# Performance work log

Measured on AMD Instinct MI355X. Metric: run time of the kernel, lower is better.

## Reference

```python
import jax, jax.numpy as jnp
import numpy as np

B, LA, LB = 16, 2048, 2048
DA, DB, DH = 768, 512, 512
EPS = 1e-5


def _layer_norm(x, g, b):
    mu = jnp.mean(x, axis=-1, keepdims=True)
    var = jnp.var(x, axis=-1, keepdims=True)
    return (x - mu) * jax.lax.rsqrt(var + EPS) * g + b


def setup_inputs() -> dict:
    key = jax.random.key(0)
    ks = jax.random.split(key, 12)
    s = lambda d: 1.0 / np.sqrt(d)
    return {
        "z_a": jax.random.normal(ks[0], (B, LA, DA), jnp.float32),
        "z_b": jax.random.normal(ks[1], (B, LB, DB), jnp.float32),
        "Wa": jax.random.uniform(ks[2], (DA, DH), jnp.float32, -s(DA), s(DA)),
        "ba": jnp.zeros((DH,), jnp.float32),
        "Wb": jax.random.uniform(ks[3], (DB, DH), jnp.float32, -s(DB), s(DB)),
        "bb": jnp.zeros((DH,), jnp.float32),
        "W_co": jax.random.normal(ks[4], (DH, DH), jnp.float32),
        "Woa": jax.random.uniform(ks[5], (DH, DA), jnp.float32, -s(DH), s(DH)),
        "boa": jnp.zeros((DA,), jnp.float32),
        "Wob": jax.random.uniform(ks[6], (DH, DB), jnp.float32, -s(DH), s(DH)),
        "bob": jnp.zeros((DB,), jnp.float32),
        "ga": jnp.ones((DA,), jnp.float32),
        "beta_a": jnp.zeros((DA,), jnp.float32),
        "gb": jnp.ones((DB,), jnp.float32),
        "beta_b": jnp.zeros((DB,), jnp.float32),
    }


def reference(z_a, z_b, Wa, ba, Wb, bb, W_co, Woa, boa, Wob, bob, ga, beta_a, gb, beta_b):
    # projections to shared hidden space
    h_a = jnp.einsum('bld,dh->blh', z_a, Wa) + ba          # (B, LA, DH)
    h_b = jnp.einsum('bld,dh->blh', z_b, Wb) + bb          # (B, LB, DH)
    # bilinear tanh co-attention scores
    C = jnp.tanh(jnp.einsum('bih,hk,bjk->bij', h_a, W_co, h_b))  # (B, LA, LB)
    attn_a = jax.nn.softmax(C, axis=-1)                    # rows: over LB
    attn_b = jax.nn.softmax(C.transpose(0, 2, 1), axis=-1) # cols: over LA
    h_a_co = jnp.einsum('bij,bjh->bih', attn_a, h_b)       # (B, LA, DH)
    h_b_co = jnp.einsum('bji,bih->bjh', attn_b, h_a)       # (B, LB, DH)
    z_a_co = jnp.einsum('blh,hd->bld', h_a_co, Woa) + boa
    z_b_co = jnp.einsum('blh,hd->bld', h_b_co, Wob) + bob
    z_a_out = _layer_norm(z_a + z_a_co, ga, beta_a)
    z_b_out = _layer_norm(z_b + z_b_co, gb, beta_b)
    return (z_a_out, z_b_out)
```

## Files before the change

kernel.cpp:

```cpp
#include <hip/hip_runtime.h>
#include <stdint.h>

typedef short bf16x8 __attribute__((ext_vector_type(8)));
typedef float f32x4 __attribute__((ext_vector_type(4)));

#define BM 256
#define BN 256
#define BK 64
#define ABUF_U 16384
#define BUF_U  32768

#define AS1 __attribute__((address_space(1)))
#define AS3 __attribute__((address_space(3)))

__device__ __forceinline__ ushort f2bf(float x) {
    uint32_t u = __float_as_uint(x);
    u += 0x7FFFu + ((u >> 16) & 1u);
    return (ushort)(u >> 16);
}

__device__ __forceinline__ void gload16(const void* g, void* l) {
    __builtin_amdgcn_global_load_lds((const AS1 void*)g, (AS3 void*)l, 16, 0, 0);
}

#define ISSUE2(kt, buf, i0)                                                          \
    do {                                                                             \
        gload16(((i0) < 4 ? Ap : Bp) + goff[i0] + (kt), smem + (buf)*BUF_U + loff[i0]); \
        gload16((((i0)+1) < 4 ? Ap : Bp) + goff[(i0)+1] + (kt), smem + (buf)*BUF_U + loff[(i0)+1]); \
    } while (0)

template<int MODE, bool HAS_BIAS, bool WRITE_T>
__global__ __launch_bounds__(512, 2)
void gemm_bt(const ushort* __restrict__ Aptr_, const ushort* __restrict__ Bptr_,
             void* __restrict__ Cptr_, ushort* __restrict__ CTptr_,
             const float* __restrict__ bias, const float* __restrict__ resid_,
             float* __restrict__ rsum_, float* __restrict__ csum_,
             const float* __restrict__ scale_,
             int M, int N, int K, int lda, int ldb, int ldc,
             long sA, long sB, long sC, long sCT, long sSum,
             int ldct, int rbshift)
{
    extern __shared__ ushort smem[];

    const int z    = blockIdx.z;
    const int m0   = blockIdx.x * BM;
    const int n0   = blockIdx.y * BN;
    const int tid  = threadIdx.x;
    const int lane = tid & 63;
    const int wave = tid >> 6;
    const int wr   = wave >> 2;
    const int wcn  = wave & 3;
    const int g    = lane >> 4, c = lane & 15;

    const ushort* Ap = Aptr_ + z * sA;
    const ushort* Bp = Bptr_ + z * sB;

    long goff[8]; int loff[8];
    #pragma unroll
    for (int u = 0; u < 4; ++u) {
        const int li  = u * 512 + tid;
        const int row = li >> 3;
        const int gck = (li & 7) ^ (row & 7);
        goff[u]     = (long)(m0 + row) * lda + gck * 8;
        loff[u]     = li * 8;
        goff[u + 4] = (long)(n0 + row) * ldb + gck * 8;
        loff[u + 4] = ABUF_U + li * 8;
    }

    f32x4 acc[8][4] = {};

    const int nk = K / BK;
    ISSUE2(0, 0, 0); ISSUE2(0, 0, 2); ISSUE2(0, 0, 4); ISSUE2(0, 0, 6);

    for (int t = 0; t < nk; ++t) {
        const int cur = t & 1, nxt = cur ^ 1;
        const ushort* As = smem + cur * BUF_U;
        const ushort* Bs = As + ABUF_U;
        const bool pf = (t + 1 < nk);
        const int kt1 = (t + 1) * BK;

        if (pf) {
            ISSUE2(kt1, nxt, 0);
            asm volatile("s_waitcnt vmcnt(2)" ::: "memory");
        } else {
            asm volatile("s_waitcnt vmcnt(0)" ::: "memory");
        }
        __builtin_amdgcn_s_barrier();

        bf16x8 af[8], bfr2[2];

        auto ldA = [&](int kk) {
            #pragma unroll
            for (int mi = 0; mi < 8; ++mi) {
                const int row = wr * 128 + mi * 16 + c;
                const int ckq = (kk * 4 + g) ^ (row & 7);
                af[mi] = *(const bf16x8*)&As[row * BK + ckq * 8];
            }
        };
        auto ldB = [&](int kk, int nh) {
            #pragma unroll
            for (int u = 0; u < 2; ++u) {
                const int row = wcn * 64 + (nh * 2 + u) * 16 + c;
                const int ckq = (kk * 4 + g) ^ (row & 7);
                bfr2[u] = *(const bf16x8*)&Bs[row * BK + ckq * 8];
            }
        };
        auto mm = [&](int nh) {
            __builtin_amdgcn_s_setprio(1);
            #pragma unroll
            for (int mi = 0; mi < 8; ++mi)
                #pragma unroll
                for (int u = 0; u < 2; ++u)
                    acc[mi][nh * 2 + u] = __builtin_amdgcn_mfma_f32_16x16x32_bf16(
                        af[mi], bfr2[u], acc[mi][nh * 2 + u], 0, 0, 0);
            __builtin_amdgcn_s_setprio(0);
        };

        ldA(0); ldB(0, 0);
        if (pf) ISSUE2(kt1, nxt, 2);
        __builtin_amdgcn_s_barrier();
        asm volatile("s_waitcnt lgkmcnt(0)" ::: "memory");
        __builtin_amdgcn_sched_barrier(0);
        mm(0);
        __builtin_amdgcn_s_barrier();
        ldB(0, 1);
        if (pf) ISSUE2(kt1, nxt, 4);
        __builtin_amdgcn_s_barrier();
        asm volatile("s_waitcnt lgkmcnt(0)" ::: "memory");
        __builtin_amdgcn_sched_barrier(0);
        mm(1);
        __builtin_amdgcn_s_barrier();
        ldA(1); ldB(1, 0);
        if (pf) ISSUE2(kt1, nxt, 6);
        __builtin_amdgcn_s_barrier();
        asm volatile("s_waitcnt lgkmcnt(0)" ::: "memory");
        __builtin_amdgcn_sched_barrier(0);
        mm(0);
        __builtin_amdgcn_s_barrier();
        ldB(1, 1);
        __builtin_amdgcn_s_barrier();
        asm volatile("s_waitcnt lgkmcnt(0)" ::: "memory");
        __builtin_amdgcn_sched_barrier(0);
        mm(1);
        __builtin_amdgcn_s_barrier();
    }

    if constexpr (MODE == 0) {
        ushort* Cp = (ushort*)Cptr_ + z * sC;
        #pragma unroll
        for (int mi = 0; mi < 8; ++mi) {
            const int row = m0 + wr * 128 + mi * 16 + g * 4;
            #pragma unroll
            for (int ni = 0; ni < 4; ++ni) {
                const int col = n0 + wcn * 64 + ni * 16 + c;
                const float bv = HAS_BIAS ? bias[col] : 0.f;
                ushort v[4];
                #pragma unroll
                for (int r = 0; r < 4; ++r) v[r] = f2bf(acc[mi][ni][r] + bv);
                #pragma unroll
                for (int r = 0; r < 4; ++r) Cp[(long)(row + r) * ldc + col] = v[r];
                if constexpr (WRITE_T) {
                    const int bb = row >> rbshift;
                    const int ii = row & ((1 << rbshift) - 1);
                    *(ushort4*)&CTptr_[(long)bb * sCT + (long)col * ldct + ii] =
                        make_ushort4(v[0], v[1], v[2], v[3]);
                }
            }
        }
    } else if constexpr (MODE == 1) {
        ushort* Ep  = (ushort*)Cptr_ + z * sC;
        ushort* ETp = CTptr_ + z * sCT;
        float* rs = rsum_ + z * sSum;
        float* cs = csum_ + z * sSum;
        float rowpart[8][4] = {};
        float colpart[4] = {};
        #pragma unroll
        for (int mi = 0; mi < 8; ++mi) {
            const int row = m0 + wr * 128 + mi * 16 + g * 4;
            #pragma unroll
            for (int ni = 0; ni < 4; ++ni) {
                const int col = n0 + wcn * 64 + ni * 16 + c;
                ushort v[4];
                #pragma unroll
                for (int r = 0; r < 4; ++r) {
                    const float s = acc[mi][ni][r];
                    const float t = 1.f - 2.f / (__expf(2.f * s) + 1.f);
                    const float e = __expf(t);
                    rowpart[mi][r] += e;
                    colpart[ni]    += e;
                    v[r] = f2bf(e);
                }
                #pragma unroll
                for (int r = 0; r < 4; ++r) Ep[(long)(row + r) * ldc + col] = v[r];
                *(ushort4*)&ETp[(long)col * ldct + row] = make_ushort4(v[0], v[1], v[2], v[3]);
            }
        }
        #pragma unroll
        for (int mi = 0; mi < 8; ++mi) {
            #pragma unroll
            for (int r = 0; r < 4; ++r) {
                float v = rowpart[mi][r];
                v += __shfl_xor(v, 1); v += __shfl_xor(v, 2);
                v += __shfl_xor(v, 4); v += __shfl_xor(v, 8);
                if (c == 0) atomicAdd(&rs[m0 + wr * 128 + mi * 16 + g * 4 + r], v);
            }
        }
        #pragma unroll
        for (int ni = 0; ni < 4; ++ni) {
            float v = colpart[ni];
            v += __shfl_xor(v, 16); v += __shfl_xor(v, 32);
            if (g == 0) atomicAdd(&cs[n0 + wcn * 64 + ni * 16 + c], v);
        }
    } else if constexpr (MODE == 2) {
        const float* sc = scale_ + z * sSum;
        ushort* Cp = (ushort*)Cptr_ + z * sC;
        #pragma unroll
        for (int mi = 0; mi < 8; ++mi) {
            const int row = m0 + wr * 128 + mi * 16 + g * 4;
            float rcp[4];
            #pragma unroll
            for (int r = 0; r < 4; ++r) rcp[r] = 1.f / sc[row + r];
            #pragma unroll
            for (int ni = 0; ni < 4; ++ni) {
                const int col = n0 + wcn * 64 + ni * 16 + c;
                #pragma unroll
                for (int r = 0; r < 4; ++r)
                    Cp[(long)(row + r) * ldc + col] = f2bf(acc[mi][ni][r] * rcp[r]);
            }
        }
    } else {
        float* Co = (float*)Cptr_;
        #pragma unroll
        for (int mi = 0; mi < 8; ++mi) {
            const int row = m0 + wr * 128 + mi * 16 + g * 4;
            #pragma unroll
            for (int ni = 0; ni < 4; ++ni) {
                const int col = n0 + wcn * 64 + ni * 16 + c;
                const float bv = bias[col];
                #pragma unroll
                for (int r = 0; r < 4; ++r) {
                    const long idx = (long)(row + r) * ldc + col;
                    Co[idx] = acc[mi][ni][r] + bv + resid_[idx];
                }
            }
        }
    }
}

__global__ __launch_bounds__(256)
void cast32to16(const float* __restrict__ in, ushort* __restrict__ out, long n) {
    const long stride = (long)gridDim.x * 256 * 8;
    for (long i = ((long)blockIdx.x * 256 + threadIdx.x) * 8; i < n; i += stride) {
        const float4 f0 = *(const float4*)(in + i);
        const float4 f1 = *(const float4*)(in + i + 4);
        uint4 w;
        w.x = (uint)f2bf(f0.x) | ((uint)f2bf(f0.y) << 16);
        w.y = (uint)f2bf(f0.z) | ((uint)f2bf(f0.w) << 16);
        w.z = (uint)f2bf(f1.x) | ((uint)f2bf(f1.y) << 16);
        w.w = (uint)f2bf(f1.z) | ((uint)f2bf(f1.w) << 16);
        *(uint4*)(out + i) = w;
    }
}

__global__ __launch_bounds__(256)
void tcast(const float* __restrict__ in, ushort* __restrict__ out, int R, int C) {
    __shared__ float t[32][33];
    const int bx = blockIdx.x * 32, by = blockIdx.y * 32;
    const int tx = threadIdx.x, ty = threadIdx.y;
    for (int i = ty; i < 32; i += 8) {
        const int r = by + i, cc = bx + tx;
        if (r < R && cc < C) t[i][tx] = in[(long)r * C + cc];
    }
    __syncthreads();
    for (int i = ty; i < 32; i += 8) {
        const int cc = bx + i, r = by + tx;
        if (cc < C && r < R) out[(long)cc * R + r] = f2bf(t[tx][i]);
    }
}

template<int D>
__global__ __launch_bounds__(256)
void ln_rows(float* __restrict__ y, const float* __restrict__ gam, const float* __restrict__ bet) {
    constexpr int NV = D / 256;
    const long row = blockIdx.x;
    float* p = y + row * D;
    const int tid = threadIdx.x;
    float v[NV];
    float s = 0.f, s2 = 0.f;
    #pragma unroll
    for (int k = 0; k < NV; ++k) {
        v[k] = p[tid + k * 256];
        s += v[k]; s2 += v[k] * v[k];
    }
    #pragma unroll
    for (int off = 1; off < 64; off <<= 1) {
        s  += __shfl_xor(s, off);
        s2 += __shfl_xor(s2, off);
    }
    __shared__ float ws[4], ws2[4];
    const int wave = tid >> 6, lane = tid & 63;
    if (lane == 0) { ws[wave] = s; ws2[wave] = s2; }
    __syncthreads();
    s  = ws[0] + ws[1] + ws[2] + ws[3];
    s2 = ws2[0] + ws2[1] + ws2[2] + ws2[3];
    const float mu  = s / D;
    const float var = s2 / D - mu * mu;
    const float rstd = rsqrtf(var + 1e-5f);
    #pragma unroll
    for (int k = 0; k < NV; ++k) {
        const int i = tid + k * 256;
        p[i] = (v[k] - mu) * rstd * gam[i] + bet[i];
    }
}

extern "C" void kernel_launch(void* const* d_in, const int* in_sizes, int n_in,
                              void* d_out, int out_size, void* d_ws, size_t ws_size,
                              hipStream_t stream)
{
    (void)in_sizes; (void)n_in; (void)out_size; (void)ws_size;
    const float* z_a    = (const float*)d_in[0];
    const float* z_b    = (const float*)d_in[1];
    const float* Wa     = (const float*)d_in[2];
    const float* ba     = (const float*)d_in[3];
    const float* Wb     = (const float*)d_in[4];
    const float* bb     = (const float*)d_in[5];
    const float* Wco    = (const float*)d_in[6];
    const float* Woa    = (const float*)d_in[7];
    const float* boa    = (const float*)d_in[8];
    const float* Wob    = (const float*)d_in[9];
    const float* bob    = (const float*)d_in[10];
    const float* ga     = (const float*)d_in[11];
    const float* beta_a = (const float*)d_in[12];
    const float* gb     = (const float*)d_in[13];
    const float* beta_b = (const float*)d_in[14];

    const int Bn = 16, LA = 2048, LB = 2048, DA = 768, DB = 512, DH = 512;
    const long MA = (long)Bn * LA;
    const long MB = (long)Bn * LB;

    char* w = (char*)d_ws;
    size_t off = 0;
    auto alc = [&](size_t bytes) { void* p = w + off; off += (bytes + 255) & ~(size_t)255; return p; };

    ushort* WaT  = (ushort*)alc((size_t)DH * DA * 2);
    ushort* WbT  = (ushort*)alc((size_t)DH * DB * 2);
    ushort* WcoT = (ushort*)alc((size_t)DH * DH * 2);
    ushort* WoaT = (ushort*)alc((size_t)DA * DH * 2);
    ushort* WobT = (ushort*)alc((size_t)DB * DH * 2);
    ushort* h_a  = (ushort*)alc((size_t)MA * DH * 2);
    ushort* h_b  = (ushort*)alc((size_t)MB * DH * 2);
    ushort* h_aT = (ushort*)alc((size_t)Bn * DH * LA * 2);
    ushort* h_bT = (ushort*)alc((size_t)Bn * DH * LB * 2);
    ushort* Ma   = (ushort*)alc((size_t)MA * DH * 2);
    ushort* E    = (ushort*)alc((size_t)Bn * LA * LB * 2);
    ushort* ET   = (ushort*)alc((size_t)Bn * LB * LA * 2);
    ushort* Pa   = (ushort*)alc((size_t)MA * DH * 2);
    ushort* Pb   = (ushort*)alc((size_t)MB * DH * 2);
    float*  rsum = (float*)alc((size_t)Bn * LA * 4);
    float*  csum = (float*)alc((size_t)Bn * LB * 4);

    ushort* za16 = E;
    ushort* zb16 = E + (size_t)MA * DA;

    dim3 blk(512, 1, 1);
    dim3 blk256(256, 1, 1);
    dim3 tb(32, 8, 1);
    const int SHM = 2 * BUF_U * 2;

    tcast<<<dim3(DH / 32, DA / 32, 1), tb, 0, stream>>>(Wa,  WaT,  DA, DH);
    tcast<<<dim3(DH / 32, DB / 32, 1), tb, 0, stream>>>(Wb,  WbT,  DB, DH);
    tcast<<<dim3(DH / 32, DH / 32, 1), tb, 0, stream>>>(Wco, WcoT, DH, DH);
    tcast<<<dim3(DA / 32, DH / 32, 1), tb, 0, stream>>>(Woa, WoaT, DH, DA);
    tcast<<<dim3(DB / 32, DH / 32, 1), tb, 0, stream>>>(Wob, WobT, DH, DB);

    cast32to16<<<dim3(2048, 1, 1), blk256, 0, stream>>>(z_a, za16, MA * DA);
    cast32to16<<<dim3(2048, 1, 1), blk256, 0, stream>>>(z_b, zb16, MB * DB);

    hipMemsetAsync(rsum, 0, (size_t)Bn * (LA + LB) * sizeof(float), stream);

    gemm_bt<0, true, true><<<dim3(MA / BM, DH / BN, 1), blk, SHM, stream>>>(
        za16, WaT, h_a, h_aT, ba, nullptr, nullptr, nullptr, nullptr,
        (int)MA, DH, DA, DA, DA, DH, 0, 0, 0, (long)DH * LA, 0, LA, 11);

    gemm_bt<0, true, true><<<dim3(MB / BM, DH / BN, 1), blk, SHM, stream>>>(
        zb16, WbT, h_b, h_bT, bb, nullptr, nullptr, nullptr, nullptr,
        (int)MB, DH, DB, DB, DB, DH, 0, 0, 0, (long)DH * LB, 0, LB, 11);

    gemm_bt<0, false, false><<<dim3(MA / BM, DH / BN, 1), blk, SHM, stream>>>(
        h_a, WcoT, Ma, nullptr, nullptr, nullptr, nullptr, nullptr, nullptr,
        (int)MA, DH, DH, DH, DH, DH, 0, 0, 0, 0, 0, 0, 0);

    gemm_bt<1, false, false><<<dim3(LA / BM, LB / BN, Bn), blk, SHM, stream>>>(
        Ma, h_b, E, ET, nullptr, nullptr, rsum, csum, nullptr,
        LA, LB, DH, DH, DH, LB,
        (long)LA * DH, (long)LB * DH, (long)LA * LB, (long)LB * LA, LA, LA, 0);

    gemm_bt<2, false, false><<<dim3(LA / BM, DH / BN, Bn), blk, SHM, stream>>>(
        E, h_bT, Pa, nullptr, nullptr, nullptr, nullptr, nullptr, rsum,
        LA, DH, LB, LB, LB, DH,
        (long)LA * LB, (long)DH * LB, (long)LA * DH, 0, LA, 0, 0);

    gemm_bt<2, false, false><<<dim3(LB / BM, DH / BN, Bn), blk, SHM, stream>>>(
        ET, h_aT, Pb, nullptr, nullptr, nullptr, nullptr, nullptr, csum,
        LB, DH, LA, LA, LA, DH,
        (long)LB * LA, (long)DH * LA, (long)LB * DH, 0, LB, 0, 0);

    float* outA = (float*)d_out;
    float* outB = outA + MA * DA;

    gemm_bt<3, true, false><<<dim3(MA / BM, DA / BN, 1), blk, SHM, stream>>>(
        Pa, WoaT, outA, nullptr, boa, z_a, nullptr, nullptr, nullptr,
        (int)MA, DA, DH, DH, DH, DA, 0, 0, 0, 0, 0, 0, 0);

    gemm_bt<3, true, false><<<dim3(MB / BM, DB / BN, 1), blk, SHM, stream>>>(
        Pb, WobT, outB, nullptr, bob, z_b, nullptr, nullptr, nullptr,
        (int)MB, DB, DH, DH, DH, DB, 0, 0, 0, 0, 0, 0, 0);

    ln_rows<768><<<dim3((unsigned)MA, 1, 1), blk256, 0, stream>>>(outA, ga, beta_a);
    ln_rows<512><<<dim3((unsigned)MB, 1, 1), blk256, 0, stream>>>(outB, gb, beta_b);
}
```

Baseline: 719.9 us.

## Stage GEMM epilogues through swizzled LDS for coalesced 16-byte global stores

All epilogue modes now write accumulator tiles into XOR-swizzled shared memory, then read them back row-contiguously and issue 16-byte vector stores. The transposed outputs are staged the same way, and the fp32 output in mode 3 uses float4 loads of bias and residual. This replaces scattered 2-byte and 4-byte global stores, including the strided transposed writes, with coalesced ones. The cost is extra LDS traffic and barriers, and the LDS buffer is reused across two halves of the tile in mode 3.

After: 726.5 us. No clear change (+0.9%).

```diff
diff --git a/kernel.cpp b/kernel.cpp
--- a/kernel.cpp
+++ b/kernel.cpp
@@ -145,103 +145,157 @@
         __builtin_amdgcn_s_barrier();
     }
 
-    if constexpr (MODE == 0) {
-        ushort* Cp = (ushort*)Cptr_ + z * sC;
+    char* img = (char*)smem;
+
+    if constexpr (MODE == 3) {
+        float* Co = (float*)Cptr_;
         #pragma unroll
-        for (int mi = 0; mi < 8; ++mi) {
-            const int row = m0 + wr * 128 + mi * 16 + g * 4;
-            #pragma unroll
-            for (int ni = 0; ni < 4; ++ni) {
-                const int col = n0 + wcn * 64 + ni * 16 + c;
-                const float bv = HAS_BIAS ? bias[col] : 0.f;
-                ushort v[4];
-                #pragma unroll
-                for (int r = 0; r < 4; ++r) v[r] = f2bf(acc[mi][ni][r] + bv);
-                #pragma unroll
-                for (int r = 0; r < 4; ++r) Cp[(long)(row + r) * ldc + col] = v[r];
-                if constexpr (WRITE_T) {
-                    const int bb = row >> rbshift;
-                    const int ii = row & ((1 << rbshift) - 1);
-                    *(ushort4*)&CTptr_[(long)bb * sCT + (long)col * ldct + ii] =
-                        make_ushort4(v[0], v[1], v[2], v[3]);
+        for (int h = 0; h < 2; ++h) {
+            if (h) __syncthreads();
+            if (wr == h) {
+                #pragma unroll
+                for (int mi = 0; mi < 8; ++mi) {
+                    const int lr0 = mi * 16 + g * 4;
+                    const int s3  = ((lr0 >> 2) & 7) << 4;
+                    #pragma unroll
+                    for (int ni = 0; ni < 4; ++ni) {
+                        const int lc4 = (wcn * 64 + ni * 16 + c) * 4;
+                        #pragma unroll
+                        for (int r = 0; r < 4; ++r)
+                            *(float*)(img + (lr0 + r) * 1024 + (lc4 ^ s3)) = acc[mi][ni][r];
+                    }
                 }
             }
-        }
-    } else if constexpr (MODE == 1) {
-        ushort* Ep  = (ushort*)Cptr_ + z * sC;
-        ushort* ETp = CTptr_ + z * sCT;
-        float* rs = rsum_ + z * sSum;
-        float* cs = csum_ + z * sSum;
+            __syncthreads();
+            #pragma unroll
+            for (int cc = 0; cc < 16; ++cc) {
+                const int ch = cc * 512 + tid;
+                const int rl = ch >> 6;
+                const int cb = (ch & 63) * 16;
+                const int s3 = ((rl >> 2) & 7) << 4;
+                float4 v = *(const float4*)(img + rl * 1024 + (cb ^ s3));
+                const int col = n0 + (ch & 63) * 4;
+                const int row = m0 + h * 128 + rl;
+                const float4 bv = *(const float4*)&bias[col];
+                const float4 rv = *(const float4*)&resid_[(long)row * ldc + col];
+                v.x += bv.x + rv.x; v.y += bv.y + rv.y;
+                v.z += bv.z + rv.z; v.w += bv.w + rv.w;
+                *(float4*)&Co[(long)row * ldc + col] = v;
+            }
+        }
+        return;
+    } else {
+        uint us[8][4][2];
         float rowpart[8][4] = {};
         float colpart[4] = {};
         #pragma unroll
         for (int mi = 0; mi < 8; ++mi) {
-            const int row = m0 + wr * 128 + mi * 16 + g * 4;
+            float rc[4];
+            if constexpr (MODE == 2) {
+                const float* sc = scale_ + z * sSum;
+                const int row = m0 + wr * 128 + mi * 16 + g * 4;
+                #pragma unroll
+                for (int r = 0; r < 4; ++r) rc[r] = 1.f / sc[row + r];
+            }
             #pragma unroll
             for (int ni = 0; ni < 4; ++ni) {
-                const int col = n0 + wcn * 64 + ni * 16 + c;
                 ushort v[4];
                 #pragma unroll
                 for (int r = 0; r < 4; ++r) {
-                    const float s = acc[mi][ni][r];
-                    const float t = 1.f - 2.f / (__expf(2.f * s) + 1.f);
-                    const float e = __expf(t);
-                    rowpart[mi][r] += e;
-                    colpart[ni]    += e;
-                    v[r] = f2bf(e);
+                    float x = acc[mi][ni][r];
+                    if constexpr (MODE == 0) {
+                        if (HAS_BIAS) x += bias[n0 + wcn * 64 + ni * 16 + c];
+                    } else if constexpr (MODE == 1) {
+                        const float th = 1.f - 2.f / (__expf(2.f * x) + 1.f);
+                        x = __expf(th);
+                        rowpart[mi][r] += x;
+                        colpart[ni]    += x;
+                    } else if constexpr (MODE == 2) {
+                        x *= rc[r];
+                    }
+                    v[r] = f2bf(x);
                 }
-                #pragma unroll
-                for (int r = 0; r < 4; ++r) Ep[(long)(row + r) * ldc + col] = v[r];
-                *(ushort4*)&ETp[(long)col * ldct + row] = make_ushort4(v[0], v[1], v[2], v[3]);
-            }
-        }
+                us[mi][ni][0] = (uint)v[0] | ((uint)v[1] << 16);
+                us[mi][ni][1] = (uint)v[2] | ((uint)v[3] << 16);
+            }
+        }
+
         #pragma unroll
         for (int mi = 0; mi < 8; ++mi) {
-            #pragma unroll
-            for (int r = 0; r < 4; ++r) {
-                float v = rowpart[mi][r];
-                v += __shfl_xor(v, 1); v += __shfl_xor(v, 2);
-                v += __shfl_xor(v, 4); v += __shfl_xor(v, 8);
-                if (c == 0) atomicAdd(&rs[m0 + wr * 128 + mi * 16 + g * 4 + r], v);
-            }
-        }
-        #pragma unroll
-        for (int ni = 0; ni < 4; ++ni) {
-            float v = colpart[ni];
-            v += __shfl_xor(v, 16); v += __shfl_xor(v, 32);
-            if (g == 0) atomicAdd(&cs[n0 + wcn * 64 + ni * 16 + c], v);
-        }
-    } else if constexpr (MODE == 2) {
-        const float* sc = scale_ + z * sSum;
-        ushort* Cp = (ushort*)Cptr_ + z * sC;
-        #pragma unroll
-        for (int mi = 0; mi < 8; ++mi) {
-            const int row = m0 + wr * 128 + mi * 16 + g * 4;
-            float rcp[4];
-            #pragma unroll
-            for (int r = 0; r < 4; ++r) rcp[r] = 1.f / sc[row + r];
+            const int lr0 = wr * 128 + mi * 16 + g * 4;
+            const int sR  = ((lr0 >> 2) & 7) << 4;
             #pragma unroll
             for (int ni = 0; ni < 4; ++ni) {
-                const int col = n0 + wcn * 64 + ni * 16 + c;
-                #pragma unroll
-                for (int r = 0; r < 4; ++r)
-                    Cp[(long)(row + r) * ldc + col] = f2bf(acc[mi][ni][r] * rcp[r]);
-            }
-        }
-    } else {
-        float* Co = (float*)Cptr_;
-        #pragma unroll
-        for (int mi = 0; mi < 8; ++mi) {
-            const int row = m0 + wr * 128 + mi * 16 + g * 4;
+                const int lc2 = (wcn * 64 + ni * 16 + c) * 2;
+                *(ushort*)(img + (lr0 + 0) * 512 + (lc2 ^ sR)) = (ushort)us[mi][ni][0];
+                *(ushort*)(img + (lr0 + 1) * 512 + (lc2 ^ sR)) = (ushort)(us[mi][ni][0] >> 16);
+                *(ushort*)(img + (lr0 + 2) * 512 + (lc2 ^ sR)) = (ushort)us[mi][ni][1];
+                *(ushort*)(img + (lr0 + 3) * 512 + (lc2 ^ sR)) = (ushort)(us[mi][ni][1] >> 16);
+            }
+        }
+        __syncthreads();
+        {
+            ushort* Cp = (ushort*)Cptr_ + z * sC;
+            #pragma unroll
+            for (int cc = 0; cc < 16; ++cc) {
+                const int ch = cc * 512 + tid;
+                const int r  = ch >> 5;
+                const int cb = (ch & 31) * 16;
+                const int sR = ((r >> 2) & 7) << 4;
+                uint4 v = *(const uint4*)(img + r * 512 + (cb ^ sR));
+                *(uint4*)((char*)Cp + ((long)(m0 + r) * ldc + n0) * 2 + cb) = v;
+            }
+        }
+
+        if constexpr (MODE == 1 || (MODE == 0 && WRITE_T)) {
+            __syncthreads();
+            #pragma unroll
+            for (int mi = 0; mi < 8; ++mi) {
+                const int lr2 = (wr * 128 + mi * 16 + g * 4) * 2;
+                #pragma unroll
+                for (int ni = 0; ni < 4; ++ni) {
+                    const int lc = wcn * 64 + ni * 16 + c;
+                    const int sT = (lc & 7) << 4;
+                    uint2 w2; w2.x = us[mi][ni][0]; w2.y = us[mi][ni][1];
+                    *(uint2*)(img + lc * 512 + (lr2 ^ sT)) = w2;
+                }
+            }
+            __syncthreads();
+            #pragma unroll
+            for (int cc = 0; cc < 16; ++cc) {
+                const int ch = cc * 512 + tid;
+                const int cl = ch >> 5;
+                const int rb = (ch & 31) * 16;
+                const int sT = (cl & 7) << 4;
+                uint4 v = *(const uint4*)(img + cl * 512 + (rb ^ sT));
+                if constexpr (MODE == 1) {
+                    *(uint4*)((char*)CTptr_ + (z * sCT + (long)(n0 + cl) * ldct + m0) * 2 + rb) = v;
+                } else {
+                    const int  bb = m0 >> rbshift;
+                    const long ii = m0 & ((1 << rbshift) - 1);
+                    *(uint4*)((char*)CTptr_ + ((long)bb * sCT + (long)(n0 + cl) * ldct + ii) * 2 + rb) = v;
+                }
+            }
+        }
+
+        if constexpr (MODE == 1) {
+            float* rs = rsum_ + z * sSum;
+            float* cs = csum_ + z * sSum;
+            #pragma unroll
+            for (int mi = 0; mi < 8; ++mi) {
+                #pragma unroll
+                for (int r = 0; r < 4; ++r) {
+                    float v = rowpart[mi][r];
+                    v += __shfl_xor(v, 1); v += __shfl_xor(v, 2);
+                    v += __shfl_xor(v, 4); v += __shfl_xor(v, 8);
+                    if (c == 0) atomicAdd(&rs[m0 + wr * 128 + mi * 16 + g * 4 + r], v);
+                }
+            }
             #pragma unroll
             for (int ni = 0; ni < 4; ++ni) {
-                const int col = n0 + wcn * 64 + ni * 16 + c;
-                const float bv = bias[col];
-                #pragma unroll
-                for (int r = 0; r < 4; ++r) {
-                    const long idx = (long)(row + r) * ldc + col;
-                    Co[idx] = acc[mi][ni][r] + bv + resid_[idx];
-                }
+                float v = colpart[ni];
+                v += __shfl_xor(v, 16); v += __shfl_xor(v, 32);
+                if (g == 0) atomicAdd(&cs[n0 + wcn * 64 + ni * 16 + c], v);
             }
         }
     }
```

## Switch GEMM to 32x32x16 MFMA tiles and add XCD-aware block remapping

Applied to the files above, without the earlier changes.

Replaces the 16x16x32 bf16 MFMA inner loop with 32x32x16 MFMA, so each wave computes 4x2 tiles of 32x32 and needs fewer LDS fragment loads per FLOP. All epilogues (bias, the exp/tanh scores with row and column sums, the normalized output, the residual output) are rewritten for the 32x32 accumulator layout. Workgroup IDs are also remapped so consecutive tiles land on the same XCD to improve L2 locality. The risks are the new row-index mapping in the epilogues and changed register pressure under the existing launch bounds of 512 threads with 2 blocks per CU.

New measurement: 713.8 us. Within noise of the previous version (-0.8%).

```diff
diff --git a/kernel.cpp b/kernel.cpp
--- a/kernel.cpp
+++ b/kernel.cpp
@@ -2,7 +2,7 @@
 #include <stdint.h>
 
 typedef short bf16x8 __attribute__((ext_vector_type(8)));
-typedef float f32x4 __attribute__((ext_vector_type(4)));
+typedef float f32x16 __attribute__((ext_vector_type(16)));
 
 #define BM 256
 #define BN 256
@@ -42,15 +42,25 @@
 {
     extern __shared__ ushort smem[];
 
-    const int z    = blockIdx.z;
-    const int m0   = blockIdx.x * BM;
-    const int n0   = blockIdx.y * BN;
+    const int gx = gridDim.x, gy = gridDim.y;
+    const int nwg = gx * gy * (int)gridDim.z;
+    int flat = ((int)blockIdx.z * gy + (int)blockIdx.y) * gx + (int)blockIdx.x;
+    {
+        const int q8 = nwg >> 3, r8 = nwg & 7;
+        const int xcd = flat & 7, loc = flat >> 3;
+        flat = (xcd < r8 ? xcd * (q8 + 1) : r8 * (q8 + 1) + (xcd - r8) * q8) + loc;
+    }
+    const int z   = flat / (gx * gy);
+    const int rem = flat - z * (gx * gy);
+    const int m0  = (rem % gx) * BM;
+    const int n0  = (rem / gx) * BN;
+
     const int tid  = threadIdx.x;
     const int lane = tid & 63;
     const int wave = tid >> 6;
     const int wr   = wave >> 2;
     const int wcn  = wave & 3;
-    const int g    = lane >> 4, c = lane & 15;
+    const int lr   = lane & 31, lh = lane >> 5;
 
     const ushort* Ap = Aptr_ + z * sA;
     const ushort* Bp = Bptr_ + z * sB;
@@ -67,7 +77,7 @@
         loff[u + 4] = ABUF_U + li * 8;
     }
 
-    f32x4 acc[8][4] = {};
+    f32x16 acc[4][2] = {};
 
     const int nk = K / BK;
     ISSUE2(0, 0, 0); ISSUE2(0, 0, 2); ISSUE2(0, 0, 4); ISSUE2(0, 0, 6);
@@ -87,161 +97,156 @@
         }
         __builtin_amdgcn_s_barrier();
 
-        bf16x8 af[8], bfr2[2];
-
-        auto ldA = [&](int kk) {
-            #pragma unroll
-            for (int mi = 0; mi < 8; ++mi) {
-                const int row = wr * 128 + mi * 16 + c;
-                const int ckq = (kk * 4 + g) ^ (row & 7);
-                af[mi] = *(const bf16x8*)&As[row * BK + ckq * 8];
-            }
-        };
-        auto ldB = [&](int kk, int nh) {
-            #pragma unroll
-            for (int u = 0; u < 2; ++u) {
-                const int row = wcn * 64 + (nh * 2 + u) * 16 + c;
-                const int ckq = (kk * 4 + g) ^ (row & 7);
-                bfr2[u] = *(const bf16x8*)&Bs[row * BK + ckq * 8];
-            }
-        };
-        auto mm = [&](int nh) {
+        bf16x8 af[4], bfv[2];
+        #pragma unroll
+        for (int kk = 0; kk < 4; ++kk) {
+            #pragma unroll
+            for (int tm = 0; tm < 4; ++tm) {
+                const int row = wr * 128 + tm * 32 + lr;
+                const int ck  = (kk * 2 + lh) ^ (row & 7);
+                af[tm] = *(const bf16x8*)&As[row * BK + ck * 8];
+            }
+            #pragma unroll
+            for (int tn = 0; tn < 2; ++tn) {
+                const int row = wcn * 64 + tn * 32 + lr;
+                const int ck  = (kk * 2 + lh) ^ (row & 7);
+                bfv[tn] = *(const bf16x8*)&Bs[row * BK + ck * 8];
+            }
+            if (pf) {
+                if (kk == 0)      ISSUE2(kt1, nxt, 2);
+                else if (kk == 1) ISSUE2(kt1, nxt, 4);
+                else if (kk == 2) ISSUE2(kt1, nxt, 6);
+            }
+            __builtin_amdgcn_s_barrier();
+            asm volatile("s_waitcnt lgkmcnt(0)" ::: "memory");
+            __builtin_amdgcn_sched_barrier(0);
             __builtin_amdgcn_s_setprio(1);
             #pragma unroll
-            for (int mi = 0; mi < 8; ++mi)
-                #pragma unroll
-                for (int u = 0; u < 2; ++u)
-                    acc[mi][nh * 2 + u] = __builtin_amdgcn_mfma_f32_16x16x32_bf16(
-                        af[mi], bfr2[u], acc[mi][nh * 2 + u], 0, 0, 0);
+            for (int tm = 0; tm < 4; ++tm)
+                #pragma unroll
+                for (int tn = 0; tn < 2; ++tn)
+                    acc[tm][tn] = __builtin_amdgcn_mfma_f32_32x32x16_bf16(
+                        af[tm], bfv[tn], acc[tm][tn], 0, 0, 0);
             __builtin_amdgcn_s_setprio(0);
-        };
-
-        ldA(0); ldB(0, 0);
-        if (pf) ISSUE2(kt1, nxt, 2);
-        __builtin_amdgcn_s_barrier();
-        asm volatile("s_waitcnt lgkmcnt(0)" ::: "memory");
-        __builtin_amdgcn_sched_barrier(0);
-        mm(0);
-        __builtin_amdgcn_s_barrier();
-        ldB(0, 1);
-        if (pf) ISSUE2(kt1, nxt, 4);
-        __builtin_amdgcn_s_barrier();
-        asm volatile("s_waitcnt lgkmcnt(0)" ::: "memory");
-        __builtin_amdgcn_sched_barrier(0);
-        mm(1);
-        __builtin_amdgcn_s_barrier();
-        ldA(1); ldB(1, 0);
-        if (pf) ISSUE2(kt1, nxt, 6);
-        __builtin_amdgcn_s_barrier();
-        asm volatile("s_waitcnt lgkmcnt(0)" ::: "memory");
-        __builtin_amdgcn_sched_barrier(0);
-        mm(0);
-        __builtin_amdgcn_s_barrier();
-        ldB(1, 1);
-        __builtin_amdgcn_s_barrier();
-        asm volatile("s_waitcnt lgkmcnt(0)" ::: "memory");
-        __builtin_amdgcn_sched_barrier(0);
-        mm(1);
-        __builtin_amdgcn_s_barrier();
-    }
-
-    if constexpr (MODE == 0) {
+            __builtin_amdgcn_s_barrier();
+        }
+    }
+
+    const int colb0 = n0 + wcn * 64 + lr;
+    const int rowbw = m0 + wr * 128 + 4 * lh;
+
+    if constexpr (MODE == 3) {
+        float* Co = (float*)Cptr_;
+        #pragma unroll
+        for (int tm = 0; tm < 4; ++tm)
+            #pragma unroll
+            for (int tn = 0; tn < 2; ++tn) {
+                const int col = colb0 + tn * 32;
+                const float bv = bias[col];
+                #pragma unroll
+                for (int q = 0; q < 4; ++q)
+                    #pragma unroll
+                    for (int s = 0; s < 4; ++s) {
+                        const int row = rowbw + tm * 32 + q * 8 + s;
+                        const long idx = (long)row * ldc + col;
+                        Co[idx] = acc[tm][tn][q * 4 + s] + bv + resid_[idx];
+                    }
+            }
+    } else if constexpr (MODE == 0) {
         ushort* Cp = (ushort*)Cptr_ + z * sC;
         #pragma unroll
-        for (int mi = 0; mi < 8; ++mi) {
-            const int row = m0 + wr * 128 + mi * 16 + g * 4;
-            #pragma unroll
-            for (int ni = 0; ni < 4; ++ni) {
-                const int col = n0 + wcn * 64 + ni * 16 + c;
+        for (int tm = 0; tm < 4; ++tm)
+            #pragma unroll
+            for (int tn = 0; tn < 2; ++tn) {
+                const int col = colb0 + tn * 32;
                 const float bv = HAS_BIAS ? bias[col] : 0.f;
-                ushort v[4];
-                #pragma unroll
-                for (int r = 0; r < 4; ++r) v[r] = f2bf(acc[mi][ni][r] + bv);
-                #pragma unroll
-                for (int r = 0; r < 4; ++r) Cp[(long)(row + r) * ldc + col] = v[r];
+                ushort us[16];
+                #pragma unroll
+                for (int rr = 0; rr < 16; ++rr) us[rr] = f2bf(acc[tm][tn][rr] + bv);
+                #pragma unroll
+                for (int q = 0; q < 4; ++q)
+                    #pragma unroll
+                    for (int s = 0; s < 4; ++s)
+                        Cp[(long)(rowbw + tm * 32 + q * 8 + s) * ldc + col] = us[q * 4 + s];
                 if constexpr (WRITE_T) {
-                    const int bb = row >> rbshift;
-                    const int ii = row & ((1 << rbshift) - 1);
-                    *(ushort4*)&CTptr_[(long)bb * sCT + (long)col * ldct + ii] =
-                        make_ushort4(v[0], v[1], v[2], v[3]);
+                    #pragma unroll
+                    for (int q = 0; q < 4; ++q) {
+                        const int gr = rowbw + tm * 32 + q * 8;
+                        const int bb = gr >> rbshift;
+                        const int ii = gr & ((1 << rbshift) - 1);
+                        *(ushort4*)&CTptr_[(long)bb * sCT + (long)col * ldct + ii] =
+                            make_ushort4(us[q * 4 + 0], us[q * 4 + 1], us[q * 4 + 2], us[q * 4 + 3]);
+                    }
                 }
             }
-        }
     } else if constexpr (MODE == 1) {
         ushort* Ep  = (ushort*)Cptr_ + z * sC;
         ushort* ETp = CTptr_ + z * sCT;
         float* rs = rsum_ + z * sSum;
         float* cs = csum_ + z * sSum;
-        float rowpart[8][4] = {};
-        float colpart[4] = {};
-        #pragma unroll
-        for (int mi = 0; mi < 8; ++mi) {
-            const int row = m0 + wr * 128 + mi * 16 + g * 4;
-            #pragma unroll
-            for (int ni = 0; ni < 4; ++ni) {
-                const int col = n0 + wcn * 64 + ni * 16 + c;
-                ushort v[4];
-                #pragma unroll
-                for (int r = 0; r < 4; ++r) {
-                    const float s = acc[mi][ni][r];
-                    const float t = 1.f - 2.f / (__expf(2.f * s) + 1.f);
-                    const float e = __expf(t);
-                    rowpart[mi][r] += e;
-                    colpart[ni]    += e;
-                    v[r] = f2bf(e);
+        float colp[2] = {0.f, 0.f};
+        #pragma unroll
+        for (int tm = 0; tm < 4; ++tm) {
+            float rowp[16];
+            #pragma unroll
+            for (int rr = 0; rr < 16; ++rr) rowp[rr] = 0.f;
+            #pragma unroll
+            for (int tn = 0; tn < 2; ++tn) {
+                const int col = colb0 + tn * 32;
+                ushort us[16];
+                #pragma unroll
+                for (int rr = 0; rr < 16; ++rr) {
+                    const float x  = acc[tm][tn][rr];
+                    const float th = 1.f - 2.f / (__expf(2.f * x) + 1.f);
+                    const float e  = __expf(th);
+                    rowp[rr] += e;
+                    colp[tn] += e;
+                    us[rr] = f2bf(e);
                 }
                 #pragma unroll
-                for (int r = 0; r < 4; ++r) Ep[(long)(row + r) * ldc + col] = v[r];
-                *(ushort4*)&ETp[(long)col * ldct + row] = make_ushort4(v[0], v[1], v[2], v[3]);
+                for (int q = 0; q < 4; ++q) {
+                    #pragma unroll
+                    for (int s = 0; s < 4; ++s)
+                        Ep[(long)(rowbw + tm * 32 + q * 8 + s) * ldc + col] = us[q * 4 + s];
+                    const int gr = rowbw + tm * 32 + q * 8;
+                    *(ushort4*)&ETp[(long)col * ldct + gr] =
+                        make_ushort4(us[q * 4 + 0], us[q * 4 + 1], us[q * 4 + 2], us[q * 4 + 3]);
+                }
+            }
+            #pragma unroll
+            for (int rr = 0; rr < 16; ++rr) {
+                float v = rowp[rr];
+                v += __shfl_xor(v, 1);  v += __shfl_xor(v, 2);
+                v += __shfl_xor(v, 4);  v += __shfl_xor(v, 8);
+                v += __shfl_xor(v, 16);
+                if (lr == 0)
+                    atomicAdd(&rs[rowbw + tm * 32 + (rr & 3) + 8 * (rr >> 2)], v);
             }
         }
         #pragma unroll
-        for (int mi = 0; mi < 8; ++mi) {
-            #pragma unroll
-            for (int r = 0; r < 4; ++r) {
-                float v = rowpart[mi][r];
-                v += __shfl_xor(v, 1); v += __shfl_xor(v, 2);
-                v += __shfl_xor(v, 4); v += __shfl_xor(v, 8);
-                if (c == 0) atomicAdd(&rs[m0 + wr * 128 + mi * 16 + g * 4 + r], v);
-            }
+        for (int tn = 0; tn < 2; ++tn) {
+            float v = colp[tn];
+            v += __shfl_xor(v, 32);
+            if (lh == 0) atomicAdd(&cs[colb0 + tn * 32], v);
         }
-        #pragma unroll
-        for (int ni = 0; ni < 4; ++ni) {
-            float v = colpart[ni];
-            v += __shfl_xor(v, 16); v += __shfl_xor(v, 32);
-            if (g == 0) atomicAdd(&cs[n0 + wcn * 64 + ni * 16 + c], v);
-        }
-    } else if constexpr (MODE == 2) {
+    } else {
         const float* sc = scale_ + z * sSum;
         ushort* Cp = (ushort*)Cptr_ + z * sC;
         #pragma unroll
-        for (int mi = 0; mi < 8; ++mi) {
-            const int row = m0 + wr * 128 + mi * 16 + g * 4;
-            float rcp[4];
-            #pragma unroll
-            for (int r = 0; r < 4; ++r) rcp[r] = 1.f / sc[row + r];
-            #pragma unroll
-            for (int ni = 0; ni < 4; ++ni) {
-                const int col = n0 + wcn * 64 + ni * 16 + c;
-                #pragma unroll
-                for (int r = 0; r < 4; ++r)
-                    Cp[(long)(row + r) * ldc + col] = f2bf(acc[mi][ni][r] * rcp[r]);
-            }
-        }
-    } else {
-        float* Co = (float*)Cptr_;
-        #pragma unroll
-        for (int mi = 0; mi < 8; ++mi) {
-            const int row = m0 + wr * 128 + mi * 16 + g * 4;
-            #pragma unroll
-            for (int ni = 0; ni < 4; ++ni) {
-                const int col = n0 + wcn * 64 + ni * 16 + c;
-                const float bv = bias[col];
-                #pragma unroll
-                for (int r = 0; r < 4; ++r) {
-                    const long idx = (long)(row + r) * ldc + col;
-                    Co[idx] = acc[mi][ni][r] + bv + resid_[idx];
-                }
+        for (int tm = 0; tm < 4; ++tm) {
+            float rcp[16];
+            #pragma unroll
+            for (int rr = 0; rr < 16; ++rr)
+                rcp[rr] = 1.f / sc[rowbw + tm * 32 + (rr & 3) + 8 * (rr >> 2)];
+            #pragma unroll
+            for (int tn = 0; tn < 2; ++tn) {
+                const int col = colb0 + tn * 32;
+                #pragma unroll
+                for (int q = 0; q < 4; ++q)
+                    #pragma unroll
+                    for (int s = 0; s < 4; ++s)
+                        Cp[(long)(rowbw + tm * 32 + q * 8 + s) * ldc + col] =
+                            f2bf(acc[tm][tn][q * 4 + s] * rcp[q * 4 + s]);
             }
         }
     }
```
